# Optimization experiments

Measured on AMD Instinct MI355X. Metric: run time of the kernel, lower is better.

Reference implementation:

```python
import math
import jax, jax.numpy as jnp
import numpy as np

N_TOKENS = 2048
HIDDEN = 2880
HEAD_DIM = 64
N_HEADS = 64
N_KV = 8
Q_MULT = N_HEADS // N_KV  # 8
SLIDING_WINDOW = 128      # layer_idx=0 -> even -> window active
RMS_EPS = 1e-5
SM_SCALE = 1.0 / math.sqrt(HEAD_DIM)
ROPE_THETA = 150000.0
INIT_CTX = 4096
SCALING_FACTOR = 32.0
NTK_ALPHA = 1.0
NTK_BETA = 32.0
QKV_DIM = HEAD_DIM * (N_HEADS + 2 * N_KV)  # 5120


def _rope_cos_sin(n_tokens):
    # YaRN/NTK-scaled inverse frequencies (scaling_factor > 1 branch)
    freq = ROPE_THETA ** (jnp.arange(0, HEAD_DIM, 2, dtype=jnp.float32) / HEAD_DIM)
    concentration = 0.1 * math.log(SCALING_FACTOR) + 1.0
    d_half = HEAD_DIM / 2
    low = d_half * math.log(INIT_CTX / (NTK_BETA * 2 * math.pi)) / math.log(ROPE_THETA)
    high = d_half * math.log(INIT_CTX / (NTK_ALPHA * 2 * math.pi)) / math.log(ROPE_THETA)
    interpolation = 1.0 / (SCALING_FACTOR * freq)
    extrapolation = 1.0 / freq
    ramp = (jnp.arange(d_half, dtype=jnp.float32) - low) / (high - low)
    mask = 1.0 - jnp.clip(ramp, 0.0, 1.0)
    inv_freq = interpolation * (1.0 - mask) + extrapolation * mask
    pos = jnp.arange(n_tokens, dtype=jnp.float32)
    freqs = pos[:, None] * inv_freq[None, :]        # [n, d/2]
    return jnp.cos(freqs) * concentration, jnp.sin(freqs) * concentration


def _apply_rotary(x, cos, sin):
    # x: [n, h, d]; cos/sin: [n, d/2]
    c = cos[:, None, :]
    s = sin[:, None, :]
    x1, x2 = jnp.split(x, 2, axis=-1)
    return jnp.concatenate([x1 * c - x2 * s, x2 * c + x1 * s], axis=-1)


def setup_inputs() -> dict:
    key = jax.random.key(0)
    ks = jax.random.split(key, 4)
    x = jax.random.normal(ks[0], (N_TOKENS, HIDDEN), dtype=jnp.float32)
    norm_scale = jnp.ones((HIDDEN,), dtype=jnp.float32)
    sinks = jax.random.normal(ks[1], (N_HEADS,), dtype=jnp.float32)
    w_qkv = jax.random.normal(ks[2], (QKV_DIM, HIDDEN), dtype=jnp.float32) * 0.02
    b_qkv = jnp.zeros((QKV_DIM,), dtype=jnp.float32)
    w_out = jax.random.normal(ks[3], (HIDDEN, N_HEADS * HEAD_DIM), dtype=jnp.float32) * 0.02
    b_out = jnp.zeros((HIDDEN,), dtype=jnp.float32)
    return {"x": x, "norm_scale": norm_scale, "sinks": sinks,
            "w_qkv": w_qkv, "b_qkv": b_qkv, "w_out": w_out, "b_out": b_out}


def reference(x, norm_scale, sinks, w_qkv, b_qkv, w_out, b_out):
    n = x.shape[0]
    # RMSNorm (fp32 math as in original)
    t = x.astype(jnp.float32)
    t = t * jax.lax.rsqrt(jnp.mean(t * t, axis=-1, keepdims=True) + RMS_EPS)
    t = (t * norm_scale).astype(x.dtype)
    # QKV projection (torch Linear: y = x @ W^T + b)
    qkv = t @ w_qkv.T + b_qkv
    q = qkv[:, : N_HEADS * HEAD_DIM].reshape(n, N_KV, Q_MULT, HEAD_DIM)
    k = qkv[:, N_HEADS * HEAD_DIM:(N_HEADS + N_KV) * HEAD_DIM].reshape(n, N_KV, HEAD_DIM)
    v = qkv[:, (N_HEADS + N_KV) * HEAD_DIM:].reshape(n, N_KV, HEAD_DIM)
    # RoPE
    cos, sin = _rope_cos_sin(n)
    q = _apply_rotary(q.reshape(n, N_HEADS, HEAD_DIM), cos, sin).reshape(n, N_KV, Q_MULT, HEAD_DIM)
    k = _apply_rotary(k, cos, sin)
    # GQA attention scores: [kv_heads, q_mult, q, k]
    qk = jnp.einsum('qhmd,khd->hmqk', q, k) * SM_SCALE
    # causal + sliding-window mask: allow j <= i and j > i - SLIDING_WINDOW
    i = jnp.arange(n)[:, None]
    j = jnp.arange(n)[None, :]
    allowed = (j <= i) & (j > i - SLIDING_WINDOW)
    neg_inf = jnp.asarray(-jnp.inf, dtype=qk.dtype)
    qk = jnp.where(allowed[None, None, :, :], qk, neg_inf)
    # append learned sink logit per head, softmax, then drop sink column
    sink_logits = jnp.broadcast_to(
        sinks.reshape(N_KV, Q_MULT, 1, 1), (N_KV, Q_MULT, n, 1)).astype(qk.dtype)
    logits = jnp.concatenate([qk, sink_logits], axis=-1)
    weights = jax.nn.softmax(logits, axis=-1)[..., :-1]
    attn = jnp.einsum('hmqk,khd->qhmd', weights, v).reshape(n, N_HEADS * HEAD_DIM)
    return x + attn @ w_out.T + b_out
```

## Files before the change

### kernel.cpp

```cpp
#include <hip/hip_runtime.h>
#include <hip/hip_bf16.h>
#include <math.h>

typedef __attribute__((ext_vector_type(8))) short short8;
typedef __attribute__((ext_vector_type(4))) float f32x4;

#define NTOK 2048
#define HID  2880
#define QKVD 5120
#define KOFF 4096
#define VOFF 4608
#define ATTD 4096

__device__ __forceinline__ unsigned short f2bf(float f) {
  union { float f; unsigned int u; } v; v.f = f;
  unsigned int u = v.u;
  unsigned int r = (u + 0x7FFFu + ((u >> 16) & 1u)) >> 16;
  return (unsigned short)r;
}
__device__ __forceinline__ float bf2f(unsigned short h) {
  union { unsigned int u; float f; } v; v.u = ((unsigned int)h) << 16; return v.f;
}
__device__ __forceinline__ void gload_lds16(const unsigned short* g, unsigned short* l) {
  __builtin_amdgcn_global_load_lds(
      (const __attribute__((address_space(1))) unsigned int*)g,
      (__attribute__((address_space(3))) unsigned int*)l, 16, 0, 0);
}
#define MFMA16(a, b, c) __builtin_amdgcn_mfma_f32_16x16x32_bf16((a), (b), (c), 0, 0, 0)

__global__ __launch_bounds__(256) void prep_kernel(
    const float* __restrict__ x, const float* __restrict__ scale,
    unsigned short* __restrict__ t,
    const float* __restrict__ w1, unsigned short* __restrict__ w1bf,
    const float* __restrict__ w2, unsigned short* __restrict__ w2bf,
    float* __restrict__ ctab, float* __restrict__ stab) {
  __shared__ float red[4];
  const int bid = blockIdx.x;
  const int tid = threadIdx.x;
  if (bid < 2048) {
    const float4* xr = (const float4*)(x + (size_t)bid * HID);
    const float4* sc = (const float4*)scale;
    float ss = 0.f;
    for (int c = tid; c < HID / 4; c += 256) {
      float4 v = xr[c];
      ss += v.x * v.x + v.y * v.y + v.z * v.z + v.w * v.w;
    }
    #pragma unroll
    for (int m = 1; m < 64; m <<= 1) ss += __shfl_xor(ss, m);
    if ((tid & 63) == 0) red[tid >> 6] = ss;
    __syncthreads();
    float tot = red[0] + red[1] + red[2] + red[3];
    float rs = rsqrtf(tot / (float)HID + 1e-5f);
    for (int c = tid; c < HID / 4; c += 256) {
      float4 v = xr[c];
      float4 s4 = sc[c];
      ushort4 o;
      o.x = f2bf(v.x * rs * s4.x); o.y = f2bf(v.y * rs * s4.y);
      o.z = f2bf(v.z * rs * s4.z); o.w = f2bf(v.w * rs * s4.w);
      *(ushort4*)&t[(size_t)bid * HID + c * 4] = o;
    }
  } else if (bid < 8528) {
    const float* src; unsigned short* dst; long base0;
    if (bid < 5648) { src = w1; dst = w1bf; base0 = (long)(bid - 2048) * 1024; }
    else            { src = w2; dst = w2bf; base0 = (long)(bid - 5648) * 1024; }
    #pragma unroll
    for (int k2 = 0; k2 < 4; ++k2) {
      long base = (base0 + k2 * 256 + tid) * 4;
      float4 v = *(const float4*)&src[base];
      ushort4 o;
      o.x = f2bf(v.x); o.y = f2bf(v.y); o.z = f2bf(v.z); o.w = f2bf(v.w);
      *(ushort4*)&dst[base] = o;
    }
  } else {
    int idx = (bid - 8528) * 256 + tid;
    int pos = idx >> 5, i = idx & 31;
    const double theta = 150000.0;
    const double two_pi = 6.283185307179586476925286766559;
    double freq = pow(theta, (double)i / 32.0);
    double interp = 1.0 / (32.0 * freq);
    double extrap = 1.0 / freq;
    double low  = 32.0 * log(4096.0 / (32.0 * two_pi)) / log(theta);
    double high = 32.0 * log(4096.0 / (1.0  * two_pi)) / log(theta);
    double ramp = ((double)i - low) / (high - low);
    ramp = ramp < 0.0 ? 0.0 : (ramp > 1.0 ? 1.0 : ramp);
    double maskv = 1.0 - ramp;
    double inv = interp * (1.0 - maskv) + extrap * maskv;
    double ang = (double)pos * inv;
    double conc = 0.1 * log(32.0) + 1.0;
    ctab[idx] = (float)(cos(ang) * conc);
    stab[idx] = (float)(sin(ang) * conc);
  }
}

template<int BN, bool RESID>
__global__ __launch_bounds__(256, 2) void gemm_kernel(
    const unsigned short* __restrict__ A, const unsigned short* __restrict__ B,
    const float* __restrict__ bias, const float* __restrict__ resid,
    void* __restrict__ Cout, int K, int NC) {
  constexpr int NF = BN / 32;
  __shared__ unsigned short sA[2][8192];
  __shared__ unsigned short sB[2][BN * 64];

  const int tid = threadIdx.x;
  const int q8 = gridDim.x >> 3;
  const int sw = ((int)blockIdx.x & 7) * q8 + ((int)blockIdx.x >> 3);
  const int m0 = (sw & 15) * 128;
  const int n0 = (sw >> 4) * BN;

  const int lane = tid & 63, wid = tid >> 6;
  const int fr = lane & 15, fq = lane >> 4;
  const int wr = wid >> 1, wc = wid & 1;
  const int swz = (fr & 7) << 4;
  const int r_st = tid >> 3;
  const int c8_st = ((tid & 7) ^ ((tid >> 3) & 7)) * 8;
  const int wlds = wid << 9;

  const unsigned short* Ag = A + (size_t)(m0 + r_st) * K + c8_st;
  const unsigned short* Bg = B + (size_t)(n0 + r_st) * K + c8_st;

  f32x4 acc[4][NF] = {};
  const int NT = K >> 6;

  auto LDA_ = [&](int bs, int mf, int ks) -> short8 {
    int row = wr * 64 + mf * 16 + fr;
    int cb = (ks * 64 + fq * 16) ^ swz;
    return *(const short8*)((const char*)&sA[bs][0] + row * 128 + cb);
  };
  auto LDB_ = [&](int bs, int nf, int ks) -> short8 {
    int row = wc * (NF * 16) + nf * 16 + fr;
    int cb = (ks * 64 + fq * 16) ^ swz;
    return *(const short8*)((const char*)&sB[bs][0] + row * 128 + cb);
  };
  auto issue_tile = [&](int tt, int b) {
    const unsigned short* Agt = Ag + (size_t)tt * 64;
    const unsigned short* Bgt = Bg + (size_t)tt * 64;
    #pragma unroll
    for (int s = 0; s < 4; ++s)
      gload_lds16(Agt + (size_t)(s * 32) * K, &sA[b][s * 2048 + wlds]);
    #pragma unroll
    for (int s = 0; s < NF; ++s)
      gload_lds16(Bgt + (size_t)(s * 32) * K, &sB[b][s * 2048 + wlds]);
  };

  issue_tile(0, 0);

  for (int t = 0; t < NT; ++t) {
    const int cu = t & 1;
    asm volatile("s_waitcnt vmcnt(0)" ::: "memory");
    __builtin_amdgcn_s_barrier();
    __builtin_amdgcn_sched_barrier(0);
    if (t + 1 < NT) issue_tile(t + 1, cu ^ 1);
    short8 afr0[4], bfr0[NF], afr1[4], bfr1[NF];
    #pragma unroll
    for (int mf = 0; mf < 4; ++mf) afr0[mf] = LDA_(cu, mf, 0);
    #pragma unroll
    for (int nf = 0; nf < NF; ++nf) bfr0[nf] = LDB_(cu, nf, 0);
    #pragma unroll
    for (int mf = 0; mf < 4; ++mf) afr1[mf] = LDA_(cu, mf, 1);
    #pragma unroll
    for (int nf = 0; nf < NF; ++nf) bfr1[nf] = LDB_(cu, nf, 1);
    __builtin_amdgcn_s_setprio(1);
    #pragma unroll
    for (int mf = 0; mf < 4; ++mf)
      #pragma unroll
      for (int nf = 0; nf < NF; ++nf)
        acc[mf][nf] = MFMA16(afr0[mf], bfr0[nf], acc[mf][nf]);
    #pragma unroll
    for (int mf = 0; mf < 4; ++mf)
      #pragma unroll
      for (int nf = 0; nf < NF; ++nf)
        acc[mf][nf] = MFMA16(afr1[mf], bfr1[nf], acc[mf][nf]);
    __builtin_amdgcn_s_setprio(0);
  }

  if (!RESID) {
    unsigned short* C = (unsigned short*)Cout;
    #pragma unroll
    for (int mf = 0; mf < 4; ++mf)
      #pragma unroll
      for (int nf = 0; nf < NF; ++nf)
        #pragma unroll
        for (int r = 0; r < 4; ++r) {
          int row = m0 + wr * 64 + mf * 16 + fq * 4 + r;
          int col = n0 + wc * (NF * 16) + nf * 16 + fr;
          C[(size_t)row * NC + col] = f2bf(acc[mf][nf][r] + bias[col]);
        }
  } else {
    float* C = (float*)Cout;
    #pragma unroll
    for (int mf = 0; mf < 4; ++mf)
      #pragma unroll
      for (int nf = 0; nf < NF; ++nf)
        #pragma unroll
        for (int r = 0; r < 4; ++r) {
          int row = m0 + wr * 64 + mf * 16 + fq * 4 + r;
          int col = n0 + wc * (NF * 16) + nf * 16 + fr;
          C[(size_t)row * NC + col] = acc[mf][nf][r] + bias[col] + resid[(size_t)row * NC + col];
        }
  }
}

__global__ __launch_bounds__(256) void attn_kernel(
    const unsigned short* __restrict__ qkv, const float* __restrict__ sinks,
    const float* __restrict__ ctab, const float* __restrict__ stab,
    unsigned short* __restrict__ attn) {
  const int tile = blockIdx.x;
  const int gh = blockIdx.y;
  const int h = gh >> 3;
  const int q0 = tile * 64;
  const int kbase = q0 - 127;

  __shared__ unsigned short Qsh[64][72];
  __shared__ unsigned short Ksh[192][72];
  __shared__ unsigned short Vt[64][200];
  __shared__ float rowpart[4][64];
  __shared__ float invsum[64];
  unsigned short (*Wsh)[200] = (unsigned short (*)[200])Ksh;

  const int tid = threadIdx.x;

  {
    int r = tid >> 2, cp = tid & 3;
    int i = q0 + r;
    const unsigned short* qp = &qkv[(size_t)i * QKVD + gh * 64 + cp * 8];
    short8 xa = *(const short8*)qp;
    short8 xb = *(const short8*)(qp + 32);
    short8 oa, ob;
    #pragma unroll
    for (int e = 0; e < 8; ++e) {
      float c = ctab[i * 32 + cp * 8 + e], s = stab[i * 32 + cp * 8 + e];
      float x1 = bf2f((unsigned short)xa[e]), x2 = bf2f((unsigned short)xb[e]);
      oa[e] = (short)f2bf(x1 * c - x2 * s);
      ob[e] = (short)f2bf(x2 * c + x1 * s);
    }
    *(short8*)&Qsh[r][cp * 8] = oa;
    *(short8*)&Qsh[r][cp * 8 + 32] = ob;
  }
  #pragma unroll
  for (int it = 0; it < 3; ++it) {
    int lin = tid + it * 256;
    int r = lin >> 2, cp = lin & 3;
    int j = kbase + r;
    short8 oa = {}, ob = {};
    if (j >= 0 && j < NTOK) {
      const unsigned short* kp = &qkv[(size_t)j * QKVD + KOFF + h * 64 + cp * 8];
      short8 xa = *(const short8*)kp;
      short8 xb = *(const short8*)(kp + 32);
      #pragma unroll
      for (int e = 0; e < 8; ++e) {
        float c = ctab[j * 32 + cp * 8 + e], s = stab[j * 32 + cp * 8 + e];
        float x1 = bf2f((unsigned short)xa[e]), x2 = bf2f((unsigned short)xb[e]);
        oa[e] = (short)f2bf(x1 * c - x2 * s);
        ob[e] = (short)f2bf(x2 * c + x1 * s);
      }
    }
    *(short8*)&Ksh[r][cp * 8] = oa;
    *(short8*)&Ksh[r][cp * 8 + 32] = ob;
  }
  {
    const int d = tid & 63;
    const int jg0 = tid >> 6;
    const unsigned short* vcol = qkv + VOFF + (size_t)h * 64 + d;
    #pragma unroll
    for (int it = 0; it < 6; ++it) {
      int jg = jg0 + it * 4;
      int jb = kbase + jg * 8;
      unsigned int e01 = 0, e23 = 0, e45 = 0, e67 = 0;
      if (jb >= 0) {
        e01 = (unsigned int)vcol[(size_t)(jb + 0) * QKVD]
            | ((unsigned int)vcol[(size_t)(jb + 1) * QKVD] << 16);
        e23 = (unsigned int)vcol[(size_t)(jb + 2) * QKVD]
            | ((unsigned int)vcol[(size_t)(jb + 3) * QKVD] << 16);
        e45 = (unsigned int)vcol[(size_t)(jb + 4) * QKVD]
            | ((unsigned int)vcol[(size_t)(jb + 5) * QKVD] << 16);
        e67 = (unsigned int)vcol[(size_t)(jb + 6) * QKVD]
            | ((unsigned int)vcol[(size_t)(jb + 7) * QKVD] << 16);
      } else if (jb + 7 >= 0) {
        unsigned short ev[8];
        #pragma unroll
        for (int e = 0; e < 8; ++e)
          ev[e] = (jb + e >= 0) ? vcol[(size_t)(jb + e) * QKVD] : (unsigned short)0;
        e01 = ev[0] | ((unsigned int)ev[1] << 16);
        e23 = ev[2] | ((unsigned int)ev[3] << 16);
        e45 = ev[4] | ((unsigned int)ev[5] << 16);
        e67 = ev[6] | ((unsigned int)ev[7] << 16);
      }
      *(uint4*)&Vt[d][jg * 8] = make_uint4(e01, e23, e45, e67);
    }
  }
  __syncthreads();

  const int lane = tid & 63;
  const int wid = tid >> 6;
  const int fr = lane & 15;
  const int fq = lane >> 4;
  const int fc = fq * 8;
  const int wk0 = wid * 48;

  f32x4 sc[4][3] = {};
  #pragma unroll
  for (int k0 = 0; k0 < 64; k0 += 32) {
    short8 qa[4], kb[3];
    #pragma unroll
    for (int mi = 0; mi < 4; ++mi) qa[mi] = *(const short8*)&Qsh[mi * 16 + fr][k0 + fc];
    #pragma unroll
    for (int ni = 0; ni < 3; ++ni) kb[ni] = *(const short8*)&Ksh[wk0 + ni * 16 + fr][k0 + fc];
    #pragma unroll
    for (int mi = 0; mi < 4; ++mi)
      #pragma unroll
      for (int ni = 0; ni < 3; ++ni)
        sc[mi][ni] = MFMA16(qa[mi], kb[ni], sc[mi][ni]);
  }

  float rsum[4][4];
  #pragma unroll
  for (int mi = 0; mi < 4; ++mi)
    #pragma unroll
    for (int r = 0; r < 4; ++r) {
      int i = q0 + mi * 16 + fq * 4 + r;
      float rs = 0.f;
      #pragma unroll
      for (int ni = 0; ni < 3; ++ni) {
        int kk = wk0 + ni * 16 + fr;
        int j = kbase + kk;
        bool valid = (j >= 0) && (j <= i) && (j > i - 128);
        float pw = valid ? __expf(sc[mi][ni][r] * 0.125f) : 0.f;
        sc[mi][ni][r] = pw;
        rs += pw;
      }
      rs += __shfl_xor(rs, 1);
      rs += __shfl_xor(rs, 2);
      rs += __shfl_xor(rs, 4);
      rs += __shfl_xor(rs, 8);
      rsum[mi][r] = rs;
    }

  __syncthreads();

  #pragma unroll
  for (int mi = 0; mi < 4; ++mi)
    #pragma unroll
    for (int r = 0; r < 4; ++r) {
      int row = mi * 16 + fq * 4 + r;
      #pragma unroll
      for (int ni = 0; ni < 3; ++ni)
        Wsh[row][wk0 + ni * 16 + fr] = f2bf(sc[mi][ni][r]);
      if (fr == 0) rowpart[wid][row] = rsum[mi][r];
    }
  __syncthreads();

  if (tid < 64) {
    float tot = rowpart[0][tid] + rowpart[1][tid] + rowpart[2][tid] + rowpart[3][tid];
    invsum[tid] = 1.f / (tot + __expf(sinks[gh]));
  }

  f32x4 pv[4] = {};
  #pragma unroll
  for (int k0 = 0; k0 < 192; k0 += 32) {
    short8 pa[4];
    #pragma unroll
    for (int mi = 0; mi < 4; ++mi) pa[mi] = *(const short8*)&Wsh[mi * 16 + fr][k0 + fc];
    short8 vb = *(const short8*)&Vt[wid * 16 + fr][k0 + fc];
    #pragma unroll
    for (int mi = 0; mi < 4; ++mi)
      pv[mi] = MFMA16(pa[mi], vb, pv[mi]);
  }
  __syncthreads();

  #pragma unroll
  for (int mi = 0; mi < 4; ++mi)
    #pragma unroll
    for (int r = 0; r < 4; ++r) {
      int row = mi * 16 + fq * 4 + r;
      float inv = invsum[row];
      int col = wid * 16 + fr;
      attn[(size_t)(q0 + row) * ATTD + gh * 64 + col] = f2bf(pv[mi][r] * inv);
    }
}

extern "C" void kernel_launch(void* const* d_in, const int* in_sizes, int n_in,
                              void* d_out, int out_size, void* d_ws, size_t ws_size,
                              hipStream_t stream) {
  const float* x          = (const float*)d_in[0];
  const float* norm_scale = (const float*)d_in[1];
  const float* sinks      = (const float*)d_in[2];
  const float* w_qkv      = (const float*)d_in[3];
  const float* b_qkv      = (const float*)d_in[4];
  const float* w_out      = (const float*)d_in[5];
  const float* b_out      = (const float*)d_in[6];
  float* out = (float*)d_out;

  char* ws = (char*)d_ws;
  unsigned short* qkv_bf = (unsigned short*)(ws);
  unsigned short* t_bf   = (unsigned short*)(ws + 20971520);
  unsigned short* attn_b = (unsigned short*)(ws + 20971520);
  unsigned short* w1bf   = (unsigned short*)(ws + 20971520 + 16777216);
  unsigned short* w2bf   = (unsigned short*)(ws + 20971520 + 16777216 + 29491200);
  float* ctab = (float*)(ws + 20971520 + 16777216 + 29491200 + 23592960);
  float* stab = ctab + NTOK * 32;

  prep_kernel<<<dim3(8784), dim3(256), 0, stream>>>(
      x, norm_scale, t_bf, w_qkv, w1bf, w_out, w2bf, ctab, stab);
  gemm_kernel<160, false><<<dim3(512), dim3(256), 0, stream>>>(
      t_bf, w1bf, b_qkv, nullptr, (void*)qkv_bf, HID, QKVD);
  attn_kernel<<<dim3(32, 64), dim3(256), 0, stream>>>(qkv_bf, sinks, ctab, stab, attn_b);
  gemm_kernel<96, true><<<dim3(480), dim3(256), 0, stream>>>(
      attn_b, w2bf, b_out, x, (void*)out, ATTD, HID);
}
```

Baseline: 196.2 us.

## Share K/V tiles across query heads within one attention block per KV head

The attention kernel now launches one 512-thread block per (query tile, KV head) and loops over the 8 query heads of the group. The roped K tile and transposed V tile are staged in LDS once and reused by all 8 heads, instead of being reloaded and recomputed by 8 separate blocks. The aim is to cut the redundant global K/V traffic and the rope work on K, especially the strided scalar V loads. In exchange the grid drops from 2048 blocks to 256, each block serialises 8 heads with extra barriers, and a separate LDS buffer for the softmax weights raises per-block shared memory.

```diff
diff --git a/kernel.cpp b/kernel.cpp
--- a/kernel.cpp
+++ b/kernel.cpp
@@ -200,70 +200,54 @@
   }
 }
 
-__global__ __launch_bounds__(256) void attn_kernel(
+__global__ __launch_bounds__(512) void attn_kernel(
     const unsigned short* __restrict__ qkv, const float* __restrict__ sinks,
     const float* __restrict__ ctab, const float* __restrict__ stab,
     unsigned short* __restrict__ attn) {
   const int tile = blockIdx.x;
-  const int gh = blockIdx.y;
-  const int h = gh >> 3;
+  const int h = blockIdx.y;
   const int q0 = tile * 64;
   const int kbase = q0 - 127;
 
   __shared__ unsigned short Qsh[64][72];
   __shared__ unsigned short Ksh[192][72];
   __shared__ unsigned short Vt[64][200];
+  __shared__ unsigned short Wsh[64][200];
   __shared__ float rowpart[4][64];
   __shared__ float invsum[64];
-  unsigned short (*Wsh)[200] = (unsigned short (*)[200])Ksh;
 
   const int tid = threadIdx.x;
 
-  {
-    int r = tid >> 2, cp = tid & 3;
-    int i = q0 + r;
-    const unsigned short* qp = &qkv[(size_t)i * QKVD + gh * 64 + cp * 8];
-    short8 xa = *(const short8*)qp;
-    short8 xb = *(const short8*)(qp + 32);
-    short8 oa, ob;
-    #pragma unroll
-    for (int e = 0; e < 8; ++e) {
-      float c = ctab[i * 32 + cp * 8 + e], s = stab[i * 32 + cp * 8 + e];
-      float x1 = bf2f((unsigned short)xa[e]), x2 = bf2f((unsigned short)xb[e]);
-      oa[e] = (short)f2bf(x1 * c - x2 * s);
-      ob[e] = (short)f2bf(x2 * c + x1 * s);
-    }
-    *(short8*)&Qsh[r][cp * 8] = oa;
-    *(short8*)&Qsh[r][cp * 8 + 32] = ob;
-  }
   #pragma unroll
-  for (int it = 0; it < 3; ++it) {
-    int lin = tid + it * 256;
-    int r = lin >> 2, cp = lin & 3;
-    int j = kbase + r;
-    short8 oa = {}, ob = {};
-    if (j >= 0 && j < NTOK) {
-      const unsigned short* kp = &qkv[(size_t)j * QKVD + KOFF + h * 64 + cp * 8];
-      short8 xa = *(const short8*)kp;
-      short8 xb = *(const short8*)(kp + 32);
-      #pragma unroll
-      for (int e = 0; e < 8; ++e) {
-        float c = ctab[j * 32 + cp * 8 + e], s = stab[j * 32 + cp * 8 + e];
-        float x1 = bf2f((unsigned short)xa[e]), x2 = bf2f((unsigned short)xb[e]);
-        oa[e] = (short)f2bf(x1 * c - x2 * s);
-        ob[e] = (short)f2bf(x2 * c + x1 * s);
+  for (int it = 0; it < 2; ++it) {
+    int lin = tid + it * 512;
+    if (lin < 768) {
+      int r = lin >> 2, cp = lin & 3;
+      int j = kbase + r;
+      short8 oa = {}, ob = {};
+      if (j >= 0 && j < NTOK) {
+        const unsigned short* kp = &qkv[(size_t)j * QKVD + KOFF + h * 64 + cp * 8];
+        short8 xa = *(const short8*)kp;
+        short8 xb = *(const short8*)(kp + 32);
+        #pragma unroll
+        for (int e = 0; e < 8; ++e) {
+          float c = ctab[j * 32 + cp * 8 + e], s = stab[j * 32 + cp * 8 + e];
+          float x1 = bf2f((unsigned short)xa[e]), x2 = bf2f((unsigned short)xb[e]);
+          oa[e] = (short)f2bf(x1 * c - x2 * s);
+          ob[e] = (short)f2bf(x2 * c + x1 * s);
+        }
       }
-    }
-    *(short8*)&Ksh[r][cp * 8] = oa;
-    *(short8*)&Ksh[r][cp * 8 + 32] = ob;
+      *(short8*)&Ksh[r][cp * 8] = oa;
+      *(short8*)&Ksh[r][cp * 8 + 32] = ob;
+    }
   }
   {
     const int d = tid & 63;
     const int jg0 = tid >> 6;
     const unsigned short* vcol = qkv + VOFF + (size_t)h * 64 + d;
     #pragma unroll
-    for (int it = 0; it < 6; ++it) {
-      int jg = jg0 + it * 4;
+    for (int it = 0; it < 3; ++it) {
+      int jg = jg0 + it * 8;
       int jb = kbase + jg * 8;
       unsigned int e01 = 0, e23 = 0, e45 = 0, e67 = 0;
       if (jb >= 0) {
@@ -288,94 +272,110 @@
       *(uint4*)&Vt[d][jg * 8] = make_uint4(e01, e23, e45, e67);
     }
   }
-  __syncthreads();
 
   const int lane = tid & 63;
   const int wid = tid >> 6;
   const int fr = lane & 15;
   const int fq = lane >> 4;
   const int fc = fq * 8;
-  const int wk0 = wid * 48;
-
-  f32x4 sc[4][3] = {};
-  #pragma unroll
-  for (int k0 = 0; k0 < 64; k0 += 32) {
-    short8 qa[4], kb[3];
-    #pragma unroll
-    for (int mi = 0; mi < 4; ++mi) qa[mi] = *(const short8*)&Qsh[mi * 16 + fr][k0 + fc];
-    #pragma unroll
-    for (int ni = 0; ni < 3; ++ni) kb[ni] = *(const short8*)&Ksh[wk0 + ni * 16 + fr][k0 + fc];
-    #pragma unroll
-    for (int mi = 0; mi < 4; ++mi)
+  const int rg = wid >> 2;
+  const int cg = wid & 3;
+  const int wk0 = cg * 48;
+
+  for (int qm = 0; qm < 8; ++qm) {
+    const int gh = h * 8 + qm;
+    if (tid < 256) {
+      int r = tid >> 2, cp = tid & 3;
+      int i = q0 + r;
+      const unsigned short* qp = &qkv[(size_t)i * QKVD + gh * 64 + cp * 8];
+      short8 xa = *(const short8*)qp;
+      short8 xb = *(const short8*)(qp + 32);
+      short8 oa, ob;
+      #pragma unroll
+      for (int e = 0; e < 8; ++e) {
+        float c = ctab[i * 32 + cp * 8 + e], s = stab[i * 32 + cp * 8 + e];
+        float x1 = bf2f((unsigned short)xa[e]), x2 = bf2f((unsigned short)xb[e]);
+        oa[e] = (short)f2bf(x1 * c - x2 * s);
+        ob[e] = (short)f2bf(x2 * c + x1 * s);
+      }
+      *(short8*)&Qsh[r][cp * 8] = oa;
+      *(short8*)&Qsh[r][cp * 8 + 32] = ob;
+    }
+    __syncthreads();
+
+    f32x4 sc[2][3] = {};
+    #pragma unroll
+    for (int k0 = 0; k0 < 64; k0 += 32) {
+      short8 qa[2], kb[3];
+      #pragma unroll
+      for (int mi = 0; mi < 2; ++mi)
+        qa[mi] = *(const short8*)&Qsh[rg * 32 + mi * 16 + fr][k0 + fc];
       #pragma unroll
       for (int ni = 0; ni < 3; ++ni)
-        sc[mi][ni] = MFMA16(qa[mi], kb[ni], sc[mi][ni]);
-  }
-
-  float rsum[4][4];
-  #pragma unroll
-  for (int mi = 0; mi < 4; ++mi)
-    #pragma unroll
-    for (int r = 0; r < 4; ++r) {
-      int i = q0 + mi * 16 + fq * 4 + r;
-      float rs = 0.f;
-      #pragma unroll
-      for (int ni = 0; ni < 3; ++ni) {
-        int kk = wk0 + ni * 16 + fr;
-        int j = kbase + kk;
-        bool valid = (j >= 0) && (j <= i) && (j > i - 128);
-        float pw = valid ? __expf(sc[mi][ni][r] * 0.125f) : 0.f;
-        sc[mi][ni][r] = pw;
-        rs += pw;
+        kb[ni] = *(const short8*)&Ksh[wk0 + ni * 16 + fr][k0 + fc];
+      #pragma unroll
+      for (int mi = 0; mi < 2; ++mi)
+        #pragma unroll
+        for (int ni = 0; ni < 3; ++ni)
+          sc[mi][ni] = MFMA16(qa[mi], kb[ni], sc[mi][ni]);
+    }
+
+    #pragma unroll
+    for (int mi = 0; mi < 2; ++mi)
+      #pragma unroll
+      for (int r = 0; r < 4; ++r) {
+        int row = rg * 32 + mi * 16 + fq * 4 + r;
+        int i = q0 + row;
+        float rs = 0.f;
+        #pragma unroll
+        for (int ni = 0; ni < 3; ++ni) {
+          int kk = wk0 + ni * 16 + fr;
+          int j = kbase + kk;
+          bool valid = (j >= 0) && (j <= i) && (j > i - 128);
+          float pw = valid ? __expf(sc[mi][ni][r] * 0.125f) : 0.f;
+          sc[mi][ni][r] = pw;
+          rs += pw;
+        }
+        rs += __shfl_xor(rs, 1);
+        rs += __shfl_xor(rs, 2);
+        rs += __shfl_xor(rs, 4);
+        rs += __shfl_xor(rs, 8);
+        #pragma unroll
+        for (int ni = 0; ni < 3; ++ni)
+          Wsh[row][wk0 + ni * 16 + fr] = f2bf(sc[mi][ni][r]);
+        if (fr == 0) rowpart[cg][row] = rs;
       }
-      rs += __shfl_xor(rs, 1);
-      rs += __shfl_xor(rs, 2);
-      rs += __shfl_xor(rs, 4);
-      rs += __shfl_xor(rs, 8);
-      rsum[mi][r] = rs;
-    }
-
-  __syncthreads();
-
-  #pragma unroll
-  for (int mi = 0; mi < 4; ++mi)
-    #pragma unroll
-    for (int r = 0; r < 4; ++r) {
-      int row = mi * 16 + fq * 4 + r;
-      #pragma unroll
-      for (int ni = 0; ni < 3; ++ni)
-        Wsh[row][wk0 + ni * 16 + fr] = f2bf(sc[mi][ni][r]);
-      if (fr == 0) rowpart[wid][row] = rsum[mi][r];
-    }
-  __syncthreads();
-
-  if (tid < 64) {
-    float tot = rowpart[0][tid] + rowpart[1][tid] + rowpart[2][tid] + rowpart[3][tid];
-    invsum[tid] = 1.f / (tot + __expf(sinks[gh]));
-  }
-
-  f32x4 pv[4] = {};
-  #pragma unroll
-  for (int k0 = 0; k0 < 192; k0 += 32) {
-    short8 pa[4];
-    #pragma unroll
-    for (int mi = 0; mi < 4; ++mi) pa[mi] = *(const short8*)&Wsh[mi * 16 + fr][k0 + fc];
-    short8 vb = *(const short8*)&Vt[wid * 16 + fr][k0 + fc];
-    #pragma unroll
-    for (int mi = 0; mi < 4; ++mi)
-      pv[mi] = MFMA16(pa[mi], vb, pv[mi]);
-  }
-  __syncthreads();
-
-  #pragma unroll
-  for (int mi = 0; mi < 4; ++mi)
-    #pragma unroll
-    for (int r = 0; r < 4; ++r) {
-      int row = mi * 16 + fq * 4 + r;
-      float inv = invsum[row];
-      int col = wid * 16 + fr;
-      attn[(size_t)(q0 + row) * ATTD + gh * 64 + col] = f2bf(pv[mi][r] * inv);
-    }
+    __syncthreads();
+
+    if (tid < 64) {
+      float tot = rowpart[0][tid] + rowpart[1][tid] + rowpart[2][tid] + rowpart[3][tid];
+      invsum[tid] = 1.f / (tot + __expf(sinks[gh]));
+    }
+
+    f32x4 pv[2] = {};
+    #pragma unroll
+    for (int k0 = 0; k0 < 192; k0 += 32) {
+      short8 pa[2];
+      #pragma unroll
+      for (int mi = 0; mi < 2; ++mi)
+        pa[mi] = *(const short8*)&Wsh[rg * 32 + mi * 16 + fr][k0 + fc];
+      short8 vb = *(const short8*)&Vt[cg * 16 + fr][k0 + fc];
+      #pragma unroll
+      for (int mi = 0; mi < 2; ++mi)
+        pv[mi] = MFMA16(pa[mi], vb, pv[mi]);
+    }
+    __syncthreads();
+
+    #pragma unroll
+    for (int mi = 0; mi < 2; ++mi)
+      #pragma unroll
+      for (int r = 0; r < 4; ++r) {
+        int row = rg * 32 + mi * 16 + fq * 4 + r;
+        float inv = invsum[row];
+        int col = cg * 16 + fr;
+        attn[(size_t)(q0 + row) * ATTD + gh * 64 + col] = f2bf(pv[mi][r] * inv);
+      }
+  }
 }
 
 extern "C" void kernel_launch(void* const* d_in, const int* in_sizes, int n_in,
@@ -403,7 +403,7 @@
       x, norm_scale, t_bf, w_qkv, w1bf, w_out, w2bf, ctab, stab);
   gemm_kernel<160, false><<<dim3(512), dim3(256), 0, stream>>>(
       t_bf, w1bf, b_qkv, nullptr, (void*)qkv_bf, HID, QKVD);
-  attn_kernel<<<dim3(32, 64), dim3(256), 0, stream>>>(qkv_bf, sinks, ctab, stab, attn_b);
+  attn_kernel<<<dim3(32, 8), dim3(512), 0, stream>>>(qkv_bf, sinks, ctab, stab, attn_b);
   gemm_kernel<96, true><<<dim3(480), dim3(256), 0, stream>>>(
       attn_b, w2bf, b_out, x, (void*)out, ATTD, HID);
 }
```

Measured after the change: 188.6 us (median of 2 runs). -3.9%, faster.
